# Performance work log

Measured on AMD Instinct MI355X. Metric: run time of the kernel, lower is better.

Reference implementation:

```python
import jax, jax.numpy as jnp
import numpy as np

B, S, HID = 2, 2048, 4096
N_HEADS, N_KV, HEAD_DIM = 32, 8, 128
N_REP = N_HEADS // N_KV
SCALING = HEAD_DIM ** -0.5
NEG_INF = -1e9


def setup_inputs() -> dict:
    key = jax.random.key(0)
    ks = jax.random.split(key, 6)
    hidden_states = jax.random.normal(ks[0], (B, S, HID), dtype=jnp.float32)
    # Real RoPE cos/sin (Llama, theta=10000): freqs repeated to full head_dim
    inv_freq = 1.0 / (10000.0 ** (jnp.arange(0, HEAD_DIM, 2, dtype=jnp.float32) / HEAD_DIM))
    pos = jnp.arange(S, dtype=jnp.float32)
    freqs = pos[:, None] * inv_freq[None, :]            # [S, HEAD_DIM//2]
    emb = jnp.concatenate([freqs, freqs], axis=-1)       # [S, HEAD_DIM]
    cos = jnp.broadcast_to(jnp.cos(emb)[None], (B, S, HEAD_DIM))
    sin = jnp.broadcast_to(jnp.sin(emb)[None], (B, S, HEAD_DIM))
    # Additive causal mask [B, 1, S, S]
    causal = jnp.triu(jnp.full((S, S), NEG_INF, dtype=jnp.float32), k=1)
    attention_mask = jnp.broadcast_to(causal[None, None], (B, 1, S, S))
    scale = 0.02
    wq = jax.random.normal(ks[1], (HID, N_HEADS * HEAD_DIM), dtype=jnp.float32) * scale
    wk = jax.random.normal(ks[2], (HID, N_KV * HEAD_DIM), dtype=jnp.float32) * scale
    wv = jax.random.normal(ks[3], (HID, N_KV * HEAD_DIM), dtype=jnp.float32) * scale
    wo = jax.random.normal(ks[4], (N_HEADS * HEAD_DIM, HID), dtype=jnp.float32) * scale
    return {"hidden_states": hidden_states, "cos": cos, "sin": sin,
            "attention_mask": attention_mask, "wq": wq, "wk": wk, "wv": wv, "wo": wo}


def _rotate_half(x):
    half = x.shape[-1] // 2
    return jnp.concatenate([-x[..., half:], x[..., :half]], axis=-1)


def reference(hidden_states, cos, sin, attention_mask, wq, wk, wv, wo):
    b, s, _ = hidden_states.shape
    # QKV projections (no bias)
    q = (hidden_states @ wq).reshape(b, s, N_HEADS, HEAD_DIM).transpose(0, 2, 1, 3)  # [b,H,s,d]
    k = (hidden_states @ wk).reshape(b, s, N_KV, HEAD_DIM).transpose(0, 2, 1, 3)     # [b,KV,s,d]
    v = (hidden_states @ wv).reshape(b, s, N_KV, HEAD_DIM).transpose(0, 2, 1, 3)
    # RoPE: broadcast cos/sin over heads (unsqueeze_dim=1)
    cos_e = cos[:, None, :, :]
    sin_e = sin[:, None, :, :]
    q = q * cos_e + _rotate_half(q) * sin_e
    k = k * cos_e + _rotate_half(k) * sin_e
    # repeat_kv: expand KV heads to match query heads
    k = jnp.repeat(k, N_REP, axis=1)  # [b,H,s,d]
    v = jnp.repeat(v, N_REP, axis=1)
    # Eager attention: full score matrix, fp32 softmax
    scores = jnp.einsum('bhqd,bhkd->bhqk', q, k) * SCALING + attention_mask
    weights = jax.nn.softmax(scores.astype(jnp.float32), axis=-1).astype(q.dtype)
    attn = jnp.einsum('bhqk,bhkd->bqhd', weights, v).reshape(b, s, N_HEADS * HEAD_DIM)
    return attn @ wo
```

## Files before the change

### kernel.cpp

```cpp
#include <hip/hip_runtime.h>
#include <hip/hip_bf16.h>

typedef __hip_bfloat16 bf16;
typedef __attribute__((ext_vector_type(8))) short short8;
typedef __attribute__((ext_vector_type(4))) float f32x4;

#define B_    2
#define S_    2048
#define HID_  4096
#define NH_   32
#define NKV_  8
#define HD_   128
#define QSTRIDE_ (NH_ * HD_)
#define QKVSTR_  6144
#define KOFF_    4096
#define VOFF_    5120
#define SCALE_ 0.08838834764831845f

__device__ __forceinline__ void lds_cp16(void* lds, const void* g) {
  __builtin_amdgcn_global_load_lds(
      (const __attribute__((address_space(1))) void*)g,
      (__attribute__((address_space(3))) void*)lds, 16, 0, 0);
}

__global__ void cvt_f32_bf16(const float* __restrict__ in, bf16* __restrict__ out,
                             long n) {
  const long i = ((long)blockIdx.x * blockDim.x + threadIdx.x) * 8;
  if (i >= n) return;
  float4 a = *(const float4*)(in + i);
  float4 b = *(const float4*)(in + i + 4);
  short8 cv;
  bf16 h;
  h = __float2bfloat16(a.x); cv[0] = *(short*)&h;
  h = __float2bfloat16(a.y); cv[1] = *(short*)&h;
  h = __float2bfloat16(a.z); cv[2] = *(short*)&h;
  h = __float2bfloat16(a.w); cv[3] = *(short*)&h;
  h = __float2bfloat16(b.x); cv[4] = *(short*)&h;
  h = __float2bfloat16(b.y); cv[5] = *(short*)&h;
  h = __float2bfloat16(b.z); cv[6] = *(short*)&h;
  h = __float2bfloat16(b.w); cv[7] = *(short*)&h;
  *(short8*)(out + i) = cv;
}

__device__ __forceinline__ void cstore(bf16* p, float v) { *p = __float2bfloat16(v); }
__device__ __forceinline__ void cstore(float* p, float v) { *p = v; }

template <typename CT>
__device__ __forceinline__ void gemm256_body(bf16* L, const bf16* __restrict__ A,
                                             const bf16* __restrict__ Bt,
                                             CT* __restrict__ C, int M, int N,
                                             int K) {
  const int tid  = threadIdx.x;
  const int wave = tid >> 6, lane = tid & 63;
  const int wm = wave >> 2, wn = wave & 3;
  const int quad = lane >> 4, l15 = lane & 15;
  const int swz  = (l15 & 7) << 3;
  const int srow = lane >> 3;
  const int scol = (((lane & 7) ^ ((lane >> 3) & 7)) << 3);

  const int nbx = N >> 8;
  const int nwg = nbx * (M >> 8);
  int wg = (int)blockIdx.y * nbx + (int)blockIdx.x;
  wg = (wg & 7) * (nwg >> 3) + (wg >> 3);
  const long m0 = (long)(wg / nbx) << 8;
  const long n0 = (long)(wg % nbx) << 8;
  const int NT = K >> 6, HT = NT << 2;

  auto STAGE = [&](int h) {
    const int t = h >> 2, idx = h & 3;
    const int isB = (idx >> 1) ^ 1;
    bf16* region = L + (t & 1) * 32768 + isB * 16384 + (idx & 1) * 8192;
    const bf16* src = isB ? Bt : A;
    const long r0 = (isB ? n0 : m0) + (idx & 1) * 128 + srow;
    const long gc = (long)t * 64 + scol;
#pragma unroll
    for (int i = 0; i < 2; ++i) {
      const int c = wave * 2 + i;
      lds_cp16(region + c * 512, src + (r0 + c * 8) * (long)K + gc);
    }
  };

  f32x4 acc[8][4] = {};
  short8 af[4][2];
  short8 bfr[2][2][2];

#pragma unroll
  for (int h = 0; h < 6; ++h) STAGE(h);
  asm volatile("s_waitcnt vmcnt(4)" ::: "memory");
  __builtin_amdgcn_s_barrier();

  auto TILE = [&](int t, int slot) {
    const int abase = slot * 32768 + wm * 8192;
    const int bbase = slot * 32768 + 16384 + (wn >> 1) * 8192 + (wn & 1) * 4096;
    const int hb = 4 * t + 6;
    const int c0 = (quad * 8) ^ swz;
    const int c1 = (32 + quad * 8) ^ swz;

#pragma unroll
    for (int m = 0; m < 4; ++m) {
      af[m][0] = *(const short8*)&L[abase + (m * 16 + l15) * 64 + c0];
      af[m][1] = *(const short8*)&L[abase + (m * 16 + l15) * 64 + c1];
    }
#pragma unroll
    for (int n = 0; n < 2; ++n) {
      bfr[0][n][0] = *(const short8*)&L[bbase + (n * 16 + l15) * 64 + c0];
      bfr[0][n][1] = *(const short8*)&L[bbase + (n * 16 + l15) * 64 + c1];
    }
    if (hb < HT) STAGE(hb);
    __builtin_amdgcn_s_barrier();
    __builtin_amdgcn_s_setprio(1);
#pragma unroll
    for (int m = 0; m < 4; ++m)
#pragma unroll
      for (int n = 0; n < 2; ++n) {
        acc[m][n] = __builtin_amdgcn_mfma_f32_16x16x32_bf16(af[m][0], bfr[0][n][0], acc[m][n], 0, 0, 0);
        acc[m][n] = __builtin_amdgcn_mfma_f32_16x16x32_bf16(af[m][1], bfr[0][n][1], acc[m][n], 0, 0, 0);
      }
    __builtin_amdgcn_s_setprio(0);
    __builtin_amdgcn_s_barrier();

#pragma unroll
    for (int n = 0; n < 2; ++n) {
      bfr[1][n][0] = *(const short8*)&L[bbase + ((n + 2) * 16 + l15) * 64 + c0];
      bfr[1][n][1] = *(const short8*)&L[bbase + ((n + 2) * 16 + l15) * 64 + c1];
    }
    if (hb + 1 < HT) STAGE(hb + 1);
    __builtin_amdgcn_s_barrier();
    __builtin_amdgcn_s_setprio(1);
#pragma unroll
    for (int m = 0; m < 4; ++m)
#pragma unroll
      for (int n = 0; n < 2; ++n) {
        acc[m][n + 2] = __builtin_amdgcn_mfma_f32_16x16x32_bf16(af[m][0], bfr[1][n][0], acc[m][n + 2], 0, 0, 0);
        acc[m][n + 2] = __builtin_amdgcn_mfma_f32_16x16x32_bf16(af[m][1], bfr[1][n][1], acc[m][n + 2], 0, 0, 0);
      }
    __builtin_amdgcn_s_setprio(0);
    __builtin_amdgcn_s_barrier();

#pragma unroll
    for (int m = 0; m < 4; ++m) {
      af[m][0] = *(const short8*)&L[abase + (64 + m * 16 + l15) * 64 + c0];
      af[m][1] = *(const short8*)&L[abase + (64 + m * 16 + l15) * 64 + c1];
    }
    if (hb + 2 < HT) STAGE(hb + 2);
    __builtin_amdgcn_s_barrier();
    __builtin_amdgcn_s_setprio(1);
#pragma unroll
    for (int m = 0; m < 4; ++m)
#pragma unroll
      for (int n = 0; n < 2; ++n) {
        acc[m + 4][n] = __builtin_amdgcn_mfma_f32_16x16x32_bf16(af[m][0], bfr[0][n][0], acc[m + 4][n], 0, 0, 0);
        acc[m + 4][n] = __builtin_amdgcn_mfma_f32_16x16x32_bf16(af[m][1], bfr[0][n][1], acc[m + 4][n], 0, 0, 0);
      }
    __builtin_amdgcn_s_setprio(0);
    __builtin_amdgcn_s_barrier();

    if (hb + 3 < HT) STAGE(hb + 3);
    __builtin_amdgcn_s_barrier();
    __builtin_amdgcn_s_setprio(1);
#pragma unroll
    for (int m = 0; m < 4; ++m)
#pragma unroll
      for (int n = 0; n < 2; ++n) {
        acc[m + 4][n + 2] = __builtin_amdgcn_mfma_f32_16x16x32_bf16(af[m][0], bfr[1][n][0], acc[m + 4][n + 2], 0, 0, 0);
        acc[m + 4][n + 2] = __builtin_amdgcn_mfma_f32_16x16x32_bf16(af[m][1], bfr[1][n][1], acc[m + 4][n + 2], 0, 0, 0);
      }
    __builtin_amdgcn_s_setprio(0);
    if (t < NT - 2) { asm volatile("s_waitcnt vmcnt(4)" ::: "memory"); }
    else            { asm volatile("s_waitcnt vmcnt(0)" ::: "memory"); }
    __builtin_amdgcn_s_barrier();
  };

#pragma unroll 1
  for (int t = 0; t < NT; t += 2) { TILE(t, 0); TILE(t + 1, 1); }

#pragma unroll
  for (int mr = 0; mr < 8; ++mr)
#pragma unroll
    for (int nr = 0; nr < 4; ++nr)
#pragma unroll
      for (int r = 0; r < 4; ++r) {
        const long row = m0 + wm * 128 + mr * 16 + quad * 4 + r;
        const long col = n0 + wn * 64 + nr * 16 + l15;
        cstore(&C[row * (long)N + col], acc[mr][nr][r]);
      }
}

__global__ __launch_bounds__(512, 2) void gemm256_bf16(
    const bf16* __restrict__ A, const bf16* __restrict__ Bt,
    bf16* __restrict__ C, int M, int N, int K) {
  __shared__ __align__(16) bf16 L[65536];
  gemm256_body<bf16>(L, A, Bt, C, M, N, K);
}

__global__ __launch_bounds__(512, 2) void gemm256_f32(
    const bf16* __restrict__ A, const bf16* __restrict__ Bt,
    float* __restrict__ C, int M, int N, int K) {
  __shared__ __align__(16) bf16 L[65536];
  gemm256_body<float>(L, A, Bt, C, M, N, K);
}

__global__ void transpose_f32_bf16(const float* __restrict__ in,
                                   bf16* __restrict__ out, int rows, int cols) {
  __shared__ bf16 t[32][33];
  const int c0 = blockIdx.x * 32, r0 = blockIdx.y * 32;
  const int tx = threadIdx.x, ty = threadIdx.y;
#pragma unroll
  for (int i = 0; i < 4; ++i)
    t[ty + i * 8][tx] =
        __float2bfloat16(in[(long)(r0 + ty + i * 8) * cols + c0 + tx]);
  __syncthreads();
#pragma unroll
  for (int i = 0; i < 4; ++i)
    out[(long)(c0 + ty + i * 8) * rows + r0 + tx] = t[tx][ty + i * 8];
}

__global__ void v_transpose(const bf16* __restrict__ QKV, bf16* __restrict__ VT) {
  __shared__ bf16 t[32][33];
  const int z = blockIdx.z;
  const int b = z >> 3, kv = z & 7;
  const int d0 = blockIdx.x * 32, s0 = blockIdx.y * 32;
  const int tx = threadIdx.x, ty = threadIdx.y;
#pragma unroll
  for (int i = 0; i < 4; ++i)
    t[ty + i * 8][tx] =
        QKV[(long)(b * S_ + s0 + ty + i * 8) * QKVSTR_ + VOFF_ + kv * HD_ + d0 + tx];
  __syncthreads();
#pragma unroll
  for (int i = 0; i < 4; ++i)
    VT[((long)z * HD_ + d0 + ty + i * 8) * S_ + s0 + tx] = t[tx][ty + i * 8];
}

__global__ void rope_kernel(bf16* __restrict__ x, const float* __restrict__ cosb,
                            const float* __restrict__ sinb, int nheads,
                            int stride, int off) {
  const int idx = blockIdx.x * blockDim.x + threadIdx.x;
  const int d  = idx & 63;
  const int h  = (idx >> 6) % nheads;
  const int bs = idx / (64 * nheads);
  if (bs >= B_ * S_) return;
  const long base = (long)bs * stride + off + h * HD_;
  const float x1 = __bfloat162float(x[base + d]);
  const float x2 = __bfloat162float(x[base + d + 64]);
  const float c1 = cosb[(long)bs * HD_ + d];
  const float c2 = cosb[(long)bs * HD_ + d + 64];
  const float s1 = sinb[(long)bs * HD_ + d];
  const float s2 = sinb[(long)bs * HD_ + d + 64];
  x[base + d]      = __float2bfloat16(x1 * c1 - x2 * s1);
  x[base + d + 64] = __float2bfloat16(x2 * c2 + x1 * s2);
}

__global__ __launch_bounds__(256, 2) void attn_fwd(const bf16* __restrict__ QKV,
                                                   const bf16* __restrict__ VT,
                                                   bf16* __restrict__ ctx) {
  __shared__ __align__(16) bf16 lK[64 * 128];
  __shared__ __align__(16) bf16 lV[128 * 64];
  __shared__ __align__(16) bf16 lP[128 * 64];
  const int tid  = threadIdx.x;
  const int wave = tid >> 6, lane = tid & 63;
  const int quad = lane >> 4, l15 = lane & 15;
  const int srow = lane >> 2, scol = (lane & 3) * 8;
  const int bh = blockIdx.y;
  const int b = bh >> 5, h = bh & 31, kv = h >> 2;
  const long qbase = (long)b * S_ * QKVSTR_ + h * HD_;
  const long kbase = (long)b * S_ * QKVSTR_ + KOFF_ + kv * HD_;
  const long vbase = (long)(b * NKV_ + kv) * HD_ * S_;
  const long cbase = (long)b * S_ * QSTRIDE_ + h * HD_;

  for (int pass = 0; pass < 2; ++pass) {
    const int qt = pass ? 15 - (int)blockIdx.x : (int)blockIdx.x;
    const int q0 = qt * 128;

    short8 qf[2][4];
#pragma unroll
    for (int mi = 0; mi < 2; ++mi)
#pragma unroll
      for (int kc = 0; kc < 4; ++kc)
        qf[mi][kc] = *(const short8*)(
            QKV + qbase + (long)(q0 + wave * 32 + mi * 16 + l15) * QKVSTR_ +
            kc * 32 + quad * 8);

    float lp[2][4] = {};
    f32x4 o[2][8] = {};

    const int nkt = 2 * qt + 2;
    for (int kt = 0; kt < nkt; ++kt) {
      const int k0 = kt * 64;
      __syncthreads();
#pragma unroll
      for (int i = 0; i < 4; ++i) {
        const int c = wave * 4 + i;
        lds_cp16(&lK[c * 512],
                 QKV + kbase + (long)(k0 + (c & 3) * 16 + srow) * QKVSTR_ +
                 (c >> 2) * 32 + scol);
        lds_cp16(&lV[c * 512],
                 VT + vbase + (long)((c & 7) * 16 + srow) * S_ + k0 +
                 (c >> 3) * 32 + scol);
      }
      __syncthreads();

      f32x4 sc[2][4] = {};
#pragma unroll
      for (int kc = 0; kc < 4; ++kc) {
        short8 kb[4];
#pragma unroll
        for (int j = 0; j < 4; ++j)
          kb[j] = *(const short8*)&lK[kc * 2048 + (j * 16 + l15) * 32 + quad * 8];
#pragma unroll
        for (int mi = 0; mi < 2; ++mi)
#pragma unroll
          for (int j = 0; j < 4; ++j)
            sc[mi][j] = __builtin_amdgcn_mfma_f32_16x16x32_bf16(
                qf[mi][kc], kb[j], sc[mi][j], 0, 0, 0);
      }

#pragma unroll
      for (int mi = 0; mi < 2; ++mi)
#pragma unroll
        for (int r = 0; r < 4; ++r) {
          const int qg = q0 + wave * 32 + mi * 16 + quad * 4 + r;
          const int rloc = wave * 32 + mi * 16 + quad * 4 + r;
#pragma unroll
          for (int j = 0; j < 4; ++j) {
            const int kg = k0 + j * 16 + l15;
            const float p = (kg <= qg) ? __expf(sc[mi][j][r] * SCALE_) : 0.f;
            lp[mi][r] += p;
            const int col = j * 16 + l15;
            lP[(col >> 5) * 4096 + rloc * 32 + (col & 31)] = __float2bfloat16(p);
          }
        }
      __syncthreads();

#pragma unroll
      for (int kc = 0; kc < 2; ++kc) {
        short8 pa[2];
#pragma unroll
        for (int mi = 0; mi < 2; ++mi)
          pa[mi] = *(const short8*)&lP[kc * 4096 + (wave * 32 + mi * 16 + l15) * 32 + quad * 8];
#pragma unroll
        for (int n = 0; n < 8; ++n) {
          const short8 vb = *(const short8*)&lV[kc * 4096 + (n * 16 + l15) * 32 + quad * 8];
#pragma unroll
          for (int mi = 0; mi < 2; ++mi)
            o[mi][n] = __builtin_amdgcn_mfma_f32_16x16x32_bf16(
                pa[mi], vb, o[mi][n], 0, 0, 0);
        }
      }
    }

#pragma unroll
    for (int mi = 0; mi < 2; ++mi)
#pragma unroll
      for (int r = 0; r < 4; ++r) {
        float l = lp[mi][r];
#pragma unroll
        for (int off = 1; off < 16; off <<= 1)
          l += __shfl_xor(l, off, 64);
        const float inv = 1.f / l;
        const long row = q0 + wave * 32 + mi * 16 + quad * 4 + r;
#pragma unroll
        for (int n = 0; n < 8; ++n)
          ctx[cbase + row * QSTRIDE_ + n * 16 + l15] =
              __float2bfloat16(o[mi][n][r] * inv);
      }
  }
}

extern "C" void kernel_launch(void* const* d_in, const int* in_sizes, int n_in,
                              void* d_out, int out_size, void* d_ws, size_t ws_size,
                              hipStream_t stream) {
  const float* hidden = (const float*)d_in[0];
  const float* cosb   = (const float*)d_in[1];
  const float* sinb   = (const float*)d_in[2];
  const float* wq = (const float*)d_in[4];
  const float* wk = (const float*)d_in[5];
  const float* wv = (const float*)d_in[6];
  const float* wo = (const float*)d_in[7];

  bf16* ws      = (bf16*)d_ws;
  bf16* hiddenB = ws;
  bf16* ctx     = ws;
  bf16* slotT   = ws + 16777216;
  bf16* VTb     = ws + 33554432;
  bf16* QKVb    = (bf16*)d_out;
  float* out    = (float*)d_out;

  const dim3 tb(32, 8);

  cvt_f32_bf16<<<8192, 256, 0, stream>>>(hidden, hiddenB, (long)B_ * S_ * HID_);

  transpose_f32_bf16<<<dim3(128, 128), tb, 0, stream>>>(wq, slotT, HID_, 4096);
  transpose_f32_bf16<<<dim3(32, 128), tb, 0, stream>>>(wk, slotT + (long)KOFF_ * HID_, HID_, 1024);
  transpose_f32_bf16<<<dim3(32, 128), tb, 0, stream>>>(wv, slotT + (long)VOFF_ * HID_, HID_, 1024);

  gemm256_bf16<<<dim3(QKVSTR_ / 256, (B_ * S_) / 256), 512, 0, stream>>>(
      hiddenB, slotT, QKVb, B_ * S_, QKVSTR_, HID_);

  rope_kernel<<<(B_ * S_ * NH_ * 64) / 256, 256, 0, stream>>>(QKVb, cosb, sinb, NH_, QKVSTR_, 0);
  rope_kernel<<<(B_ * S_ * NKV_ * 64) / 256, 256, 0, stream>>>(QKVb, cosb, sinb, NKV_, QKVSTR_, KOFF_);

  v_transpose<<<dim3(4, 64, B_ * NKV_), tb, 0, stream>>>(QKVb, VTb);

  attn_fwd<<<dim3(8, B_ * NH_), 256, 0, stream>>>(QKVb, VTb, ctx);

  transpose_f32_bf16<<<dim3(128, 128), tb, 0, stream>>>(wo, slotT, QSTRIDE_, HID_);
  gemm256_f32<<<dim3(HID_ / 256, (B_ * S_) / 256), 512, 0, stream>>>(
      ctx, slotT, out, B_ * S_, HID_, HID_);
}
```

Before: 727.3 us.

## Double-buffer K/V tiles in attention and swizzle P layout in LDS

After: 722.5 us. About the same (-0.7%).

```diff
diff --git a/kernel.cpp b/kernel.cpp
--- a/kernel.cpp
+++ b/kernel.cpp
@@ -253,13 +253,14 @@
 __global__ __launch_bounds__(256, 2) void attn_fwd(const bf16* __restrict__ QKV,
                                                    const bf16* __restrict__ VT,
                                                    bf16* __restrict__ ctx) {
-  __shared__ __align__(16) bf16 lK[64 * 128];
-  __shared__ __align__(16) bf16 lV[128 * 64];
-  __shared__ __align__(16) bf16 lP[128 * 64];
+  __shared__ __align__(16) bf16 lK[2][8192];
+  __shared__ __align__(16) bf16 lV[2][8192];
+  __shared__ __align__(16) bf16 lP[8192];
   const int tid  = threadIdx.x;
   const int wave = tid >> 6, lane = tid & 63;
   const int quad = lane >> 4, l15 = lane & 15;
   const int srow = lane >> 2, scol = (lane & 3) * 8;
+  const int rkey = (l15 >> 2) & 3;
   const int bh = blockIdx.y;
   const int b = bh >> 5, h = bh & 31, kv = h >> 2;
   const long qbase = (long)b * S_ * QKVSTR_ + h * HD_;
@@ -267,6 +268,20 @@
   const long vbase = (long)(b * NKV_ + kv) * HD_ * S_;
   const long cbase = (long)b * S_ * QSTRIDE_ + h * HD_;
 
+  auto STAGE = [&](int kt, int buf) {
+    const int k0s = kt * 64;
+#pragma unroll
+    for (int i = 0; i < 4; ++i) {
+      const int c = wave * 4 + i;
+      lds_cp16(&lK[buf][c * 512],
+               QKV + kbase + (long)(k0s + (c & 3) * 16 + srow) * QKVSTR_ +
+               (c >> 2) * 32 + scol);
+      lds_cp16(&lV[buf][c * 512],
+               VT + vbase + (long)((c & 7) * 16 + srow) * S_ + k0s +
+               (c >> 3) * 32 + scol);
+    }
+  };
+
   for (int pass = 0; pass < 2; ++pass) {
     const int qt = pass ? 15 - (int)blockIdx.x : (int)blockIdx.x;
     const int q0 = qt * 128;
@@ -283,29 +298,28 @@
     float lp[2][4] = {};
     f32x4 o[2][8] = {};
 
+    int cur = 0;
     const int nkt = 2 * qt + 2;
     for (int kt = 0; kt < nkt; ++kt) {
       const int k0 = kt * 64;
-      __syncthreads();
-#pragma unroll
-      for (int i = 0; i < 4; ++i) {
-        const int c = wave * 4 + i;
-        lds_cp16(&lK[c * 512],
-                 QKV + kbase + (long)(k0 + (c & 3) * 16 + srow) * QKVSTR_ +
-                 (c >> 2) * 32 + scol);
-        lds_cp16(&lV[c * 512],
-                 VT + vbase + (long)((c & 7) * 16 + srow) * S_ + k0 +
-                 (c >> 3) * 32 + scol);
-      }
-      __syncthreads();
+      __builtin_amdgcn_s_barrier();
+      if (kt == 0) STAGE(0, 0);
+      if (kt + 1 < nkt) {
+        STAGE(kt + 1, cur ^ 1);
+        asm volatile("s_waitcnt vmcnt(8)" ::: "memory");
+      } else {
+        asm volatile("s_waitcnt vmcnt(0)" ::: "memory");
+      }
+      __builtin_amdgcn_s_barrier();
 
       f32x4 sc[2][4] = {};
+      __builtin_amdgcn_s_setprio(1);
 #pragma unroll
       for (int kc = 0; kc < 4; ++kc) {
         short8 kb[4];
 #pragma unroll
         for (int j = 0; j < 4; ++j)
-          kb[j] = *(const short8*)&lK[kc * 2048 + (j * 16 + l15) * 32 + quad * 8];
+          kb[j] = *(const short8*)&lK[cur][kc * 2048 + (j * 16 + l15) * 32 + quad * 8];
 #pragma unroll
         for (int mi = 0; mi < 2; ++mi)
 #pragma unroll
@@ -313,6 +327,7 @@
             sc[mi][j] = __builtin_amdgcn_mfma_f32_16x16x32_bf16(
                 qf[mi][kc], kb[j], sc[mi][j], 0, 0, 0);
       }
+      __builtin_amdgcn_s_setprio(0);
 
 #pragma unroll
       for (int mi = 0; mi < 2; ++mi)
@@ -325,27 +340,34 @@
             const int kg = k0 + j * 16 + l15;
             const float p = (kg <= qg) ? __expf(sc[mi][j][r] * SCALE_) : 0.f;
             lp[mi][r] += p;
-            const int col = j * 16 + l15;
-            lP[(col >> 5) * 4096 + rloc * 32 + (col & 31)] = __float2bfloat16(p);
+            const int cc = (j & 1) * 16 + l15;
+            const int slot = ((cc >> 3) ^ quad) & 3;
+            lP[(j >> 1) * 4096 + rloc * 32 + slot * 8 + (cc & 7)] =
+                __float2bfloat16(p);
           }
         }
-      __syncthreads();
-
+      asm volatile("s_waitcnt lgkmcnt(0)" ::: "memory");
+      __builtin_amdgcn_s_barrier();
+
+      __builtin_amdgcn_s_setprio(1);
 #pragma unroll
       for (int kc = 0; kc < 2; ++kc) {
         short8 pa[2];
 #pragma unroll
         for (int mi = 0; mi < 2; ++mi)
-          pa[mi] = *(const short8*)&lP[kc * 4096 + (wave * 32 + mi * 16 + l15) * 32 + quad * 8];
+          pa[mi] = *(const short8*)&lP[kc * 4096 + (wave * 32 + mi * 16 + l15) * 32 +
+                                       ((quad ^ rkey) & 3) * 8];
 #pragma unroll
         for (int n = 0; n < 8; ++n) {
-          const short8 vb = *(const short8*)&lV[kc * 4096 + (n * 16 + l15) * 32 + quad * 8];
+          const short8 vb = *(const short8*)&lV[cur][kc * 4096 + (n * 16 + l15) * 32 + quad * 8];
 #pragma unroll
           for (int mi = 0; mi < 2; ++mi)
             o[mi][n] = __builtin_amdgcn_mfma_f32_16x16x32_bf16(
                 pa[mi], vb, o[mi][n], 0, 0, 0);
         }
       }
+      __builtin_amdgcn_s_setprio(0);
+      cur ^= 1;
     }
 
 #pragma unroll
```
